# Kernel optimization log

Measured on AMD Instinct MI355X. Metric: run time of the kernel, lower is better.

Reference implementation:

```python
import jax, jax.numpy as jnp
import numpy as np

B, N, K, F_IN, F_OUT = 8, 2048, 32, 256, 256


def setup_inputs() -> dict:
    key = jax.random.key(0)
    ks = jax.random.split(key, 8)
    x = jax.random.normal(ks[0], (B, N, F_IN), dtype=jnp.float32)
    idx_neib = jax.random.randint(ks[1], (N, K), 0, N, dtype=jnp.int32)
    # Linear params (torch nn.Linear stores weight as [out, in])
    lim_x = np.sqrt(2.0) * np.sqrt(6.0 / (F_IN + F_OUT))  # xavier_uniform, gain=relu
    Wx_w = jax.random.uniform(ks[2], (F_OUT, F_IN), jnp.float32, -lim_x, lim_x)
    Wx_b = jnp.zeros((F_OUT,), jnp.float32)
    Wn_w = jax.random.uniform(ks[3], (F_OUT, F_IN), jnp.float32, -lim_x, lim_x)
    Wn_b = jnp.zeros((F_OUT,), jnp.float32)
    gamma = jnp.ones((2 * F_OUT,), jnp.float32)
    beta = jnp.zeros((2 * F_OUT,), jnp.float32)
    return {"x": x, "idx_neib": idx_neib, "Wx_w": Wx_w, "Wx_b": Wx_b,
            "Wn_w": Wn_w, "Wn_b": Wn_b, "gamma": gamma, "beta": beta}


def reference(x, idx_neib, Wx_w, Wx_b, Wn_w, Wn_b, gamma, beta):
    # Gather neighbor features: [B, N, K, F] then mean over the K neighbors.
    x_neib = jnp.take(x, idx_neib, axis=1).mean(axis=2)  # [B, N, F]
    # Dual linear projections (weights stored [out, in] as in torch).
    h_self = jnp.einsum('bnf,of->bno', x, Wx_w) + Wx_b
    h_nei = jnp.einsum('bnf,of->bno', x_neib, Wn_w) + Wn_b
    h = jnp.concatenate([h_self, h_nei], axis=2)          # [B, N, 2*out]
    # F.normalize(p=2, dim=2): divide by max(||h||_2, 1e-12)
    nrm = jnp.sqrt(jnp.sum(h * h, axis=2, keepdims=True))
    h = h / jnp.maximum(nrm, 1e-12)
    h = jax.nn.relu(h)
    # BatchNorm1d over channel dim (training mode: batch stats over B and N,
    # biased variance), eps=1e-5.
    mu = h.mean(axis=(0, 1))
    var = jnp.mean((h - mu) ** 2, axis=(0, 1))
    h = (h - mu) * jax.lax.rsqrt(var + 1e-5) * gamma + beta
    return h
```

## Files before the change

kernel.cpp:

```cpp
#include <hip/hip_runtime.h>
#include <stdint.h>

#define BB 8
#define NN 2048
#define KK 32
#define FIN 256
#define FOUT 256
#define CC 512
#define MM (BB*NN)
#define RB 32
#define NBLK (MM/RB)
#define LDA 264

typedef __attribute__((ext_vector_type(8))) short short8;
typedef __attribute__((ext_vector_type(4))) float f32x4;
typedef __attribute__((ext_vector_type(2))) float f32x2;

__device__ __forceinline__ unsigned short f2bf(float f) {
    union { float f; unsigned u; } v; v.f = f;
    unsigned u = v.u;
    return (unsigned short)((u + 0x7FFFu + ((u >> 16) & 1u)) >> 16);
}
__device__ __forceinline__ float bf2f(unsigned short s) {
    union { unsigned u; float f; } v; v.u = ((unsigned)s) << 16;
    return v.f;
}
__device__ __forceinline__ f32x2 bfpair(unsigned u) {
    union { unsigned u; float f; } lo, hi;
    lo.u = u << 16;
    hi.u = u & 0xFFFF0000u;
    return (f32x2){lo.f, hi.f};
}

__global__ void k_prep(const float* __restrict__ Wx, const float* __restrict__ Wxb,
                       const float* __restrict__ Wn, const float* __restrict__ Wnb,
                       const float* __restrict__ x,
                       unsigned short* __restrict__ Wc, float* __restrict__ bc,
                       unsigned short* __restrict__ xb) {
    const int blk = blockIdx.x;
    const int tid = threadIdx.x;
    if (blk < 128) {
        int gid = blk * 256 + tid;
        int e0 = gid * 4;
        int o = e0 >> 8, k = e0 & 255;
        const float* src = (o < FOUT) ? (Wx + o * FIN + k) : (Wn + (o - FOUT) * FIN + k);
        float4 v = *(const float4*)src;
        ushort4 p; p.x = f2bf(v.x); p.y = f2bf(v.y); p.z = f2bf(v.z); p.w = f2bf(v.w);
        *(ushort4*)(Wc + e0) = p;
        if (gid < 128) {
            int c0 = gid * 4;
            float4 bv = (c0 < FOUT) ? *(const float4*)(Wxb + c0)
                                    : *(const float4*)(Wnb + c0 - FOUT);
            *(float4*)(bc + c0) = bv;
        }
    } else {
        size_t gid = (size_t)(blk - 128) * 256 + tid;
        size_t e0 = gid * 8;
        float4 v0 = *(const float4*)(x + e0);
        float4 v1 = *(const float4*)(x + e0 + 4);
        ushort4 p0, p1;
        p0.x = f2bf(v0.x); p0.y = f2bf(v0.y); p0.z = f2bf(v0.z); p0.w = f2bf(v0.w);
        p1.x = f2bf(v1.x); p1.y = f2bf(v1.y); p1.z = f2bf(v1.z); p1.w = f2bf(v1.w);
        *(ushort4*)(xb + e0)     = p0;
        *(ushort4*)(xb + e0 + 4) = p1;
    }
}

__global__ __launch_bounds__(512, 4)
void k_gemm(const unsigned short* __restrict__ xb, const int* __restrict__ idx,
            const unsigned short* __restrict__ Wc,
            const float* __restrict__ bc,
            unsigned short* __restrict__ h,
            float* __restrict__ psum, float* __restrict__ psq) {
    __shared__ unsigned short As[2][RB * LDA];
    __shared__ float sqpart[8][RB];
    __shared__ float rnorm[RB];

    const int bid  = blockIdx.x;
    const int tid  = threadIdx.x;
    const int w    = tid >> 6;
    const int lane = tid & 63;
    const int quad = lane >> 4;
    const int l16  = lane & 15;
    const int p    = lane >> 5;
    const int l32  = lane & 31;
    const int b    = bid & 7;
    const int n0   = (bid >> 3) * RB;
    const unsigned short* xbat = xb + (size_t)b * NN * FIN;
    const size_t r0g = (size_t)b * NN + n0;

    {
        const uint4* gs = (const uint4*)(xbat + (size_t)n0 * FIN);
        #pragma unroll
        for (int i = 0; i < 2; ++i) {
            int e = tid + i * 512;
            *(uint4*)&As[0][(e >> 5) * LDA + (e & 31) * 8] = gs[e];
        }
    }
    {
        const int* ip = idx + (n0 + (w << 2)) * KK;
        const unsigned short* xp = xbat + l32 * 8;
        f32x2 ac[4][4];
        #pragma unroll
        for (int rr = 0; rr < 4; ++rr)
            #pragma unroll
            for (int c = 0; c < 4; ++c) ac[rr][c] = (f32x2){0.f, 0.f};

        #pragma unroll 2
        for (int k = 0; k < 16; ++k) {
            int kk = (k << 1) | p;
            int j0 = ip[0 * KK + kk];
            int j1 = ip[1 * KK + kk];
            int j2 = ip[2 * KK + kk];
            int j3 = ip[3 * KK + kk];
            uint4 v0 = *(const uint4*)(xp + (size_t)j0 * FIN);
            uint4 v1 = *(const uint4*)(xp + (size_t)j1 * FIN);
            uint4 v2 = *(const uint4*)(xp + (size_t)j2 * FIN);
            uint4 v3 = *(const uint4*)(xp + (size_t)j3 * FIN);
            const unsigned* u0 = (const unsigned*)&v0;
            const unsigned* u1 = (const unsigned*)&v1;
            const unsigned* u2 = (const unsigned*)&v2;
            const unsigned* u3 = (const unsigned*)&v3;
            #pragma unroll
            for (int c = 0; c < 4; ++c) {
                ac[0][c] += bfpair(u0[c]);
                ac[1][c] += bfpair(u1[c]);
                ac[2][c] += bfpair(u2[c]);
                ac[3][c] += bfpair(u3[c]);
            }
        }
        const float s = 1.0f / (float)KK;
        #pragma unroll
        for (int rr = 0; rr < 4; ++rr) {
            #pragma unroll
            for (int c = 0; c < 4; ++c) {
                ac[rr][c][0] += __shfl_xor(ac[rr][c][0], 32, 64);
                ac[rr][c][1] += __shfl_xor(ac[rr][c][1], 32, 64);
            }
            if (p == 0) {
                unsigned short o8[8];
                #pragma unroll
                for (int c = 0; c < 4; ++c) {
                    o8[2 * c]     = f2bf(ac[rr][c][0] * s);
                    o8[2 * c + 1] = f2bf(ac[rr][c][1] * s);
                }
                *(uint4*)&As[1][((w << 2) + rr) * LDA + l32 * 8] = *(const uint4*)o8;
            }
        }
    }
    __syncthreads();

    const int half = w >> 2;
    const unsigned short* A = As[half];
    const int cbg = half * 256 + (w & 3) * 64;

    f32x4 acc[2][4];
    #pragma unroll
    for (int mt = 0; mt < 2; ++mt)
        #pragma unroll
        for (int nt = 0; nt < 4; ++nt) acc[mt][nt] = (f32x4){0.f, 0.f, 0.f, 0.f};

    const unsigned short* Bp = Wc + (size_t)(cbg + l16) * FIN + quad * 8;
    const unsigned short* Ap = A + (size_t)l16 * LDA + quad * 8;

    #pragma unroll 2
    for (int k0 = 0; k0 < FIN; k0 += 32) {
        short8 a0 = *(const short8*)(Ap + k0);
        short8 a1 = *(const short8*)(Ap + 16 * LDA + k0);
        short8 bfr[4];
        #pragma unroll
        for (int nt = 0; nt < 4; ++nt)
            bfr[nt] = *(const short8*)(Bp + (size_t)nt * 16 * FIN + k0);
        #pragma unroll
        for (int nt = 0; nt < 4; ++nt) {
            acc[0][nt] = __builtin_amdgcn_mfma_f32_16x16x32_bf16(a0, bfr[nt], acc[0][nt], 0, 0, 0);
            acc[1][nt] = __builtin_amdgcn_mfma_f32_16x16x32_bf16(a1, bfr[nt], acc[1][nt], 0, 0, 0);
        }
    }

    float bcv[4];
    #pragma unroll
    for (int nt = 0; nt < 4; ++nt) bcv[nt] = bc[cbg + nt * 16 + l16];

    float rsq[2][4] = {{0.f,0.f,0.f,0.f},{0.f,0.f,0.f,0.f}};
    #pragma unroll
    for (int mt = 0; mt < 2; ++mt)
        #pragma unroll
        for (int nt = 0; nt < 4; ++nt)
            #pragma unroll
            for (int r = 0; r < 4; ++r) {
                float v = acc[mt][nt][r] + bcv[nt];
                acc[mt][nt][r] = v;
                rsq[mt][r] += v * v;
            }
    #pragma unroll
    for (int off = 1; off < 16; off <<= 1)
        #pragma unroll
        for (int mt = 0; mt < 2; ++mt)
            #pragma unroll
            for (int r = 0; r < 4; ++r)
                rsq[mt][r] += __shfl_xor(rsq[mt][r], off, 64);
    if (l16 == 0) {
        #pragma unroll
        for (int mt = 0; mt < 2; ++mt)
            #pragma unroll
            for (int r = 0; r < 4; ++r)
                sqpart[w][mt * 16 + quad * 4 + r] = rsq[mt][r];
    }
    __syncthreads();
    if (tid < RB) {
        float tot = 0.f;
        #pragma unroll
        for (int i = 0; i < 8; ++i) tot += sqpart[i][tid];
        rnorm[tid] = 1.0f / fmaxf(sqrtf(tot), 1e-12f);
    }
    __syncthreads();

    float csum[4] = {0.f,0.f,0.f,0.f};
    float csq [4] = {0.f,0.f,0.f,0.f};
    #pragma unroll
    for (int mt = 0; mt < 2; ++mt) {
        #pragma unroll
        for (int r = 0; r < 4; ++r) {
            int row = mt * 16 + quad * 4 + r;
            float rn = rnorm[row];
            unsigned short* hp = h + (r0g + row) * CC + cbg + l16;
            #pragma unroll
            for (int nt = 0; nt < 4; ++nt) {
                float v = fmaxf(acc[mt][nt][r] * rn, 0.0f);
                hp[nt * 16] = f2bf(v);
                csum[nt] += v;
                csq [nt] += v * v;
            }
        }
    }
    #pragma unroll
    for (int off = 16; off < 64; off <<= 1)
        #pragma unroll
        for (int nt = 0; nt < 4; ++nt) {
            csum[nt] += __shfl_xor(csum[nt], off, 64);
            csq [nt] += __shfl_xor(csq [nt], off, 64);
        }
    if (quad == 0 && p == 0) {
        #pragma unroll
        for (int nt = 0; nt < 4; ++nt) {
            int c = cbg + nt * 16 + l16;
            psum[(size_t)c * NBLK + bid] = csum[nt];
            psq [(size_t)c * NBLK + bid] = csq [nt];
        }
    }
}

__global__ void k_stats(const float* __restrict__ psum, const float* __restrict__ psq,
                        const float* __restrict__ gamma, const float* __restrict__ beta,
                        float* __restrict__ ss) {
    __shared__ float ps[4], pq[4];
    int c = blockIdx.x, t = threadIdx.x;
    float s = psum[(size_t)c * NBLK + t] + psum[(size_t)c * NBLK + 256 + t];
    float q = psq [(size_t)c * NBLK + t] + psq [(size_t)c * NBLK + 256 + t];
    #pragma unroll
    for (int off = 32; off; off >>= 1) { s += __shfl_xor(s, off, 64); q += __shfl_xor(q, off, 64); }
    int w = t >> 6, lane = t & 63;
    if (lane == 0) { ps[w] = s; pq[w] = q; }
    __syncthreads();
    if (t == 0) {
        float S = ps[0] + ps[1] + ps[2] + ps[3];
        float Q = pq[0] + pq[1] + pq[2] + pq[3];
        const float inv = 1.0f / (float)MM;
        float mu  = S * inv;
        float var = fmaxf(Q * inv - mu * mu, 0.0f);
        float sc  = gamma[c] * rsqrtf(var + 1e-5f);
        ss[c]      = sc;
        ss[CC + c] = beta[c] - mu * sc;
    }
}

__global__ void k_apply(const unsigned short* __restrict__ h,
                        const float* __restrict__ ss,
                        float* __restrict__ out) {
    int gid = blockIdx.x * 256 + threadIdx.x;
    int c0 = (gid * 8) & (CC - 1);
    uint4 hv = ((const uint4*)h)[gid];
    const unsigned short* hs = (const unsigned short*)&hv;
    float4 sc0 = *(const float4*)(ss + c0);
    float4 sc1 = *(const float4*)(ss + c0 + 4);
    float4 sh0 = *(const float4*)(ss + CC + c0);
    float4 sh1 = *(const float4*)(ss + CC + c0 + 4);
    float4 o0, o1;
    o0.x = bf2f(hs[0]) * sc0.x + sh0.x;
    o0.y = bf2f(hs[1]) * sc0.y + sh0.y;
    o0.z = bf2f(hs[2]) * sc0.z + sh0.z;
    o0.w = bf2f(hs[3]) * sc0.w + sh0.w;
    o1.x = bf2f(hs[4]) * sc1.x + sh1.x;
    o1.y = bf2f(hs[5]) * sc1.y + sh1.y;
    o1.z = bf2f(hs[6]) * sc1.z + sh1.z;
    o1.w = bf2f(hs[7]) * sc1.w + sh1.w;
    ((float4*)out)[gid * 2]     = o0;
    ((float4*)out)[gid * 2 + 1] = o1;
}

extern "C" void kernel_launch(void* const* d_in, const int* in_sizes, int n_in,
                              void* d_out, int out_size, void* d_ws, size_t ws_size,
                              hipStream_t stream) {
    const float* x     = (const float*)d_in[0];
    const int*   idx   = (const int*)  d_in[1];
    const float* Wx_w  = (const float*)d_in[2];
    const float* Wx_b  = (const float*)d_in[3];
    const float* Wn_w  = (const float*)d_in[4];
    const float* Wn_b  = (const float*)d_in[5];
    const float* gamma = (const float*)d_in[6];
    const float* beta  = (const float*)d_in[7];
    float* out = (float*)d_out;

    char* p = (char*)d_ws;
    unsigned short* xb = (unsigned short*)p; p += (size_t)MM * FIN * 2;
    unsigned short* Wc = (unsigned short*)p; p += (size_t)CC * FIN * 2;
    float* bc          = (float*)p;          p += (size_t)CC * 4;
    unsigned short* h  = (unsigned short*)p; p += (size_t)MM * CC * 2;
    float* psum        = (float*)p;          p += (size_t)CC * NBLK * 4;
    float* psq         = (float*)p;          p += (size_t)CC * NBLK * 4;
    float* ss          = (float*)p;          p += (size_t)2 * CC * 4;

    hipLaunchKernelGGL(k_prep,  dim3(2176), dim3(256), 0, stream,
                       Wx_w, Wx_b, Wn_w, Wn_b, x, Wc, bc, xb);
    hipLaunchKernelGGL(k_gemm,  dim3(NBLK), dim3(512), 0, stream, xb, idx, Wc, bc, h, psum, psq);
    hipLaunchKernelGGL(k_stats, dim3(CC),   dim3(256), 0, stream, psum, psq, gamma, beta, ss);
    hipLaunchKernelGGL(k_apply, dim3(4096), dim3(256), 0, stream, h, ss, out);
}
```

Baseline: 129.1 us.

## Fuse GEMM, batchnorm stats and apply into one persistent kernel with grid barriers

Merges the gemm, stats and apply kernels into one kernel of 256 blocks of 1024 threads, each handling 64 rows as two 32-row groups. Activations stay in registers across two software grid barriers, so the bf16 intermediate h is never written to or read back from global memory, and two kernel launches disappear. The stats reduction is spread over blocks, two channels per block. The risks are that the spin barrier needs all 256 blocks to be co-resident, since a deadlock would only end at the iteration cap, and that 1024-thread blocks lower occupancy during the gather and GEMM.

```diff
diff --git a/kernel.cpp b/kernel.cpp
--- a/kernel.cpp
+++ b/kernel.cpp
@@ -9,7 +9,8 @@
 #define CC 512
 #define MM (BB*NN)
 #define RB 32
-#define NBLK (MM/RB)
+#define NBLK 256
+#define NPART 512
 #define LDA 264
 
 typedef __attribute__((ext_vector_type(8))) short short8;
@@ -20,10 +21,6 @@
     union { float f; unsigned u; } v; v.f = f;
     unsigned u = v.u;
     return (unsigned short)((u + 0x7FFFu + ((u >> 16) & 1u)) >> 16);
-}
-__device__ __forceinline__ float bf2f(unsigned short s) {
-    union { unsigned u; float f; } v; v.u = ((unsigned)s) << 16;
-    return v.f;
 }
 __device__ __forceinline__ f32x2 bfpair(unsigned u) {
     union { unsigned u; float f; } lo, hi;
@@ -32,14 +29,29 @@
     return (f32x2){lo.f, hi.f};
 }
 
+__device__ __forceinline__ void gbar(unsigned* c) {
+    __syncthreads();
+    if (threadIdx.x == 0) {
+        __hip_atomic_fetch_add(c, 1u, __ATOMIC_ACQ_REL, __HIP_MEMORY_SCOPE_AGENT);
+        int t = 0;
+        while (__hip_atomic_load(c, __ATOMIC_ACQUIRE, __HIP_MEMORY_SCOPE_AGENT)
+                   < (unsigned)NBLK && ++t < 5000000) {
+            __builtin_amdgcn_s_sleep(2);
+        }
+    }
+    __syncthreads();
+}
+
 __global__ void k_prep(const float* __restrict__ Wx, const float* __restrict__ Wxb,
                        const float* __restrict__ Wn, const float* __restrict__ Wnb,
                        const float* __restrict__ x,
                        unsigned short* __restrict__ Wc, float* __restrict__ bc,
-                       unsigned short* __restrict__ xb) {
+                       unsigned short* __restrict__ xb, unsigned* __restrict__ bar) {
     const int blk = blockIdx.x;
     const int tid = threadIdx.x;
     if (blk < 128) {
+        if (blk == 0 && tid < 2)
+            __hip_atomic_store(&bar[tid], 0u, __ATOMIC_RELAXED, __HIP_MEMORY_SCOPE_AGENT);
         int gid = blk * 256 + tid;
         int e0 = gid * 4;
         int o = e0 >> 8, k = e0 & 255;
@@ -66,39 +78,44 @@
     }
 }
 
-__global__ __launch_bounds__(512, 4)
-void k_gemm(const unsigned short* __restrict__ xb, const int* __restrict__ idx,
-            const unsigned short* __restrict__ Wc,
-            const float* __restrict__ bc,
-            unsigned short* __restrict__ h,
-            float* __restrict__ psum, float* __restrict__ psq) {
-    __shared__ unsigned short As[2][RB * LDA];
-    __shared__ float sqpart[8][RB];
-    __shared__ float rnorm[RB];
+__global__ __launch_bounds__(1024, 4)
+void k_fused(const unsigned short* __restrict__ xb, const int* __restrict__ idx,
+             const unsigned short* __restrict__ Wc,
+             const float* __restrict__ bc,
+             const float* __restrict__ gamma, const float* __restrict__ beta,
+             float* __restrict__ psum, float* __restrict__ psq,
+             float* __restrict__ ss, unsigned* __restrict__ bar,
+             float* __restrict__ out) {
+    __shared__ unsigned short As[2][2][RB * LDA];
+    __shared__ float sqpart[2][8][RB];
+    __shared__ float rnorm[2][RB];
+    __shared__ float red[32];
 
     const int bid  = blockIdx.x;
     const int tid  = threadIdx.x;
     const int w    = tid >> 6;
+    const int g    = w >> 3;
+    const int wl   = w & 7;
     const int lane = tid & 63;
     const int quad = lane >> 4;
     const int l16  = lane & 15;
     const int p    = lane >> 5;
     const int l32  = lane & 31;
     const int b    = bid & 7;
-    const int n0   = (bid >> 3) * RB;
+    const int n0   = (bid >> 3) * (2 * RB);
     const unsigned short* xbat = xb + (size_t)b * NN * FIN;
-    const size_t r0g = (size_t)b * NN + n0;
+    const size_t r0g = (size_t)b * NN + n0 + (g << 5);
 
     {
         const uint4* gs = (const uint4*)(xbat + (size_t)n0 * FIN);
         #pragma unroll
         for (int i = 0; i < 2; ++i) {
-            int e = tid + i * 512;
-            *(uint4*)&As[0][(e >> 5) * LDA + (e & 31) * 8] = gs[e];
+            int e = tid + i * 1024;
+            *(uint4*)&As[e >> 10][0][((e >> 5) & 31) * LDA + (e & 31) * 8] = gs[e];
         }
     }
     {
-        const int* ip = idx + (n0 + (w << 2)) * KK;
+        const int* ip = idx + (n0 + (g << 5) + (wl << 2)) * KK;
         const unsigned short* xp = xbat + l32 * 8;
         f32x2 ac[4][4];
         #pragma unroll
@@ -144,15 +161,15 @@
                     o8[2 * c]     = f2bf(ac[rr][c][0] * s);
                     o8[2 * c + 1] = f2bf(ac[rr][c][1] * s);
                 }
-                *(uint4*)&As[1][((w << 2) + rr) * LDA + l32 * 8] = *(const uint4*)o8;
-            }
-        }
-    }
-    __syncthreads();
-
-    const int half = w >> 2;
-    const unsigned short* A = As[half];
-    const int cbg = half * 256 + (w & 3) * 64;
+                *(uint4*)&As[g][1][((wl << 2) + rr) * LDA + l32 * 8] = *(const uint4*)o8;
+            }
+        }
+    }
+    __syncthreads();
+
+    const int half = wl >> 2;
+    const unsigned short* A = As[g][half];
+    const int cbg = half * 256 + (wl & 3) * 64;
 
     f32x4 acc[2][4];
     #pragma unroll
@@ -205,14 +222,15 @@
         for (int mt = 0; mt < 2; ++mt)
             #pragma unroll
             for (int r = 0; r < 4; ++r)
-                sqpart[w][mt * 16 + quad * 4 + r] = rsq[mt][r];
-    }
-    __syncthreads();
-    if (tid < RB) {
+                sqpart[g][wl][mt * 16 + quad * 4 + r] = rsq[mt][r];
+    }
+    __syncthreads();
+    if (tid < 2 * RB) {
+        int gg = tid >> 5, row = tid & 31;
         float tot = 0.f;
         #pragma unroll
-        for (int i = 0; i < 8; ++i) tot += sqpart[i][tid];
-        rnorm[tid] = 1.0f / fmaxf(sqrtf(tot), 1e-12f);
+        for (int i = 0; i < 8; ++i) tot += sqpart[gg][i][row];
+        rnorm[gg][row] = 1.0f / fmaxf(sqrtf(tot), 1e-12f);
     }
     __syncthreads();
 
@@ -223,12 +241,11 @@
         #pragma unroll
         for (int r = 0; r < 4; ++r) {
             int row = mt * 16 + quad * 4 + r;
-            float rn = rnorm[row];
-            unsigned short* hp = h + (r0g + row) * CC + cbg + l16;
+            float rn = rnorm[g][row];
             #pragma unroll
             for (int nt = 0; nt < 4; ++nt) {
                 float v = fmaxf(acc[mt][nt][r] * rn, 0.0f);
-                hp[nt * 16] = f2bf(v);
+                acc[mt][nt][r] = v;
                 csum[nt] += v;
                 csq [nt] += v * v;
             }
@@ -241,62 +258,63 @@
             csum[nt] += __shfl_xor(csum[nt], off, 64);
             csq [nt] += __shfl_xor(csq [nt], off, 64);
         }
-    if (quad == 0 && p == 0) {
+    if (quad == 0) {
         #pragma unroll
         for (int nt = 0; nt < 4; ++nt) {
             int c = cbg + nt * 16 + l16;
-            psum[(size_t)c * NBLK + bid] = csum[nt];
-            psq [(size_t)c * NBLK + bid] = csq [nt];
-        }
-    }
-}
-
-__global__ void k_stats(const float* __restrict__ psum, const float* __restrict__ psq,
-                        const float* __restrict__ gamma, const float* __restrict__ beta,
-                        float* __restrict__ ss) {
-    __shared__ float ps[4], pq[4];
-    int c = blockIdx.x, t = threadIdx.x;
-    float s = psum[(size_t)c * NBLK + t] + psum[(size_t)c * NBLK + 256 + t];
-    float q = psq [(size_t)c * NBLK + t] + psq [(size_t)c * NBLK + 256 + t];
-    #pragma unroll
-    for (int off = 32; off; off >>= 1) { s += __shfl_xor(s, off, 64); q += __shfl_xor(q, off, 64); }
-    int w = t >> 6, lane = t & 63;
-    if (lane == 0) { ps[w] = s; pq[w] = q; }
-    __syncthreads();
-    if (t == 0) {
-        float S = ps[0] + ps[1] + ps[2] + ps[3];
-        float Q = pq[0] + pq[1] + pq[2] + pq[3];
-        const float inv = 1.0f / (float)MM;
-        float mu  = S * inv;
-        float var = fmaxf(Q * inv - mu * mu, 0.0f);
-        float sc  = gamma[c] * rsqrtf(var + 1e-5f);
-        ss[c]      = sc;
-        ss[CC + c] = beta[c] - mu * sc;
-    }
-}
-
-__global__ void k_apply(const unsigned short* __restrict__ h,
-                        const float* __restrict__ ss,
-                        float* __restrict__ out) {
-    int gid = blockIdx.x * 256 + threadIdx.x;
-    int c0 = (gid * 8) & (CC - 1);
-    uint4 hv = ((const uint4*)h)[gid];
-    const unsigned short* hs = (const unsigned short*)&hv;
-    float4 sc0 = *(const float4*)(ss + c0);
-    float4 sc1 = *(const float4*)(ss + c0 + 4);
-    float4 sh0 = *(const float4*)(ss + CC + c0);
-    float4 sh1 = *(const float4*)(ss + CC + c0 + 4);
-    float4 o0, o1;
-    o0.x = bf2f(hs[0]) * sc0.x + sh0.x;
-    o0.y = bf2f(hs[1]) * sc0.y + sh0.y;
-    o0.z = bf2f(hs[2]) * sc0.z + sh0.z;
-    o0.w = bf2f(hs[3]) * sc0.w + sh0.w;
-    o1.x = bf2f(hs[4]) * sc1.x + sh1.x;
-    o1.y = bf2f(hs[5]) * sc1.y + sh1.y;
-    o1.z = bf2f(hs[6]) * sc1.z + sh1.z;
-    o1.w = bf2f(hs[7]) * sc1.w + sh1.w;
-    ((float4*)out)[gid * 2]     = o0;
-    ((float4*)out)[gid * 2 + 1] = o1;
+            psum[(size_t)c * NPART + (bid << 1) + g] = csum[nt];
+            psq [(size_t)c * NPART + (bid << 1) + g] = csq [nt];
+        }
+    }
+
+    gbar(bar + 0);
+
+    {
+        const int hh   = tid >> 9;
+        const int ch   = (bid << 1) | hh;
+        const int part = tid & 511;
+        float s = psum[(size_t)ch * NPART + part];
+        float q = psq [(size_t)ch * NPART + part];
+        #pragma unroll
+        for (int off = 32; off; off >>= 1) {
+            s += __shfl_xor(s, off, 64);
+            q += __shfl_xor(q, off, 64);
+        }
+        if (lane == 0) { red[w] = s; red[16 + w] = q; }
+        __syncthreads();
+        if (part == 0) {
+            float S = 0.f, Q = 0.f;
+            #pragma unroll
+            for (int i = 0; i < 8; ++i) { S += red[hh * 8 + i]; Q += red[16 + hh * 8 + i]; }
+            const float inv = 1.0f / (float)MM;
+            float mu  = S * inv;
+            float var = fmaxf(Q * inv - mu * mu, 0.0f);
+            float sc  = gamma[ch] * rsqrtf(var + 1e-5f);
+            ss[ch]      = sc;
+            ss[CC + ch] = beta[ch] - mu * sc;
+        }
+    }
+
+    gbar(bar + 1);
+
+    float scv[4], shv[4];
+    #pragma unroll
+    for (int nt = 0; nt < 4; ++nt) {
+        int c = cbg + nt * 16 + l16;
+        scv[nt] = ss[c];
+        shv[nt] = ss[CC + c];
+    }
+    #pragma unroll
+    for (int mt = 0; mt < 2; ++mt) {
+        #pragma unroll
+        for (int r = 0; r < 4; ++r) {
+            int row = mt * 16 + quad * 4 + r;
+            float* op = out + (r0g + row) * CC + cbg + l16;
+            #pragma unroll
+            for (int nt = 0; nt < 4; ++nt)
+                op[nt * 16] = fmaf(acc[mt][nt][r], scv[nt], shv[nt]);
+        }
+    }
 }
 
 extern "C" void kernel_launch(void* const* d_in, const int* in_sizes, int n_in,
@@ -316,14 +334,13 @@
     unsigned short* xb = (unsigned short*)p; p += (size_t)MM * FIN * 2;
     unsigned short* Wc = (unsigned short*)p; p += (size_t)CC * FIN * 2;
     float* bc          = (float*)p;          p += (size_t)CC * 4;
-    unsigned short* h  = (unsigned short*)p; p += (size_t)MM * CC * 2;
-    float* psum        = (float*)p;          p += (size_t)CC * NBLK * 4;
-    float* psq         = (float*)p;          p += (size_t)CC * NBLK * 4;
+    float* psum        = (float*)p;          p += (size_t)CC * NPART * 4;
+    float* psq         = (float*)p;          p += (size_t)CC * NPART * 4;
     float* ss          = (float*)p;          p += (size_t)2 * CC * 4;
-
-    hipLaunchKernelGGL(k_prep,  dim3(2176), dim3(256), 0, stream,
-                       Wx_w, Wx_b, Wn_w, Wn_b, x, Wc, bc, xb);
-    hipLaunchKernelGGL(k_gemm,  dim3(NBLK), dim3(512), 0, stream, xb, idx, Wc, bc, h, psum, psq);
-    hipLaunchKernelGGL(k_stats, dim3(CC),   dim3(256), 0, stream, psum, psq, gamma, beta, ss);
-    hipLaunchKernelGGL(k_apply, dim3(4096), dim3(256), 0, stream, h, ss, out);
-}
+    unsigned* bar      = (unsigned*)p;       p += 2 * sizeof(unsigned);
+
+    hipLaunchKernelGGL(k_prep, dim3(2176), dim3(256), 0, stream,
+                       Wx_w, Wx_b, Wn_w, Wn_b, x, Wc, bc, xb, bar);
+    hipLaunchKernelGGL(k_fused, dim3(NBLK), dim3(1024), 0, stream,
+                       xb, idx, Wc, bc, gamma, beta, psum, psq, ss, bar, out);
+}
```

After: 173.3 us. 1.34x slower.
